# Performance work log

Hardware: AMD Instinct MI355X
Metric: run time of the kernel (lower is better)

## Reference

```python
import jax, jax.numpy as jnp
import numpy as np

DIM = 768
NUM_HEADS = 12
HEAD_DIM = DIM // NUM_HEADS
SCALE = HEAD_DIM ** -0.5
ELEV_SCALE = 1000.0


def setup_inputs() -> dict:
    key = jax.random.key(0)
    ks = jax.random.split(key, 6)
    B, N = 2, 2048
    x = jax.random.normal(ks[0], (B, N, DIM), dtype=jnp.float32)
    # elevation in meters, roughly 0..3000 m
    elevation_patches = jax.random.uniform(ks[1], (B, N), dtype=jnp.float32) * 3000.0
    # torch nn.Linear weights are [out, in]; y = x @ W.T + b
    w_qkv = jax.random.normal(ks[2], (3 * DIM, DIM), dtype=jnp.float32) * (DIM ** -0.5)
    w_proj = jax.random.normal(ks[3], (DIM, DIM), dtype=jnp.float32) * (DIM ** -0.5)
    b_proj = jax.random.normal(ks[4], (DIM,), dtype=jnp.float32) * 0.02
    alpha = jnp.ones((1,), dtype=jnp.float32)
    return {"x": x, "elevation_patches": elevation_patches,
            "w_qkv": w_qkv, "w_proj": w_proj, "b_proj": b_proj, "alpha": alpha}


def _elevation_bias(elev, alpha):
    # elev: [B, N] -> bias [B, N, N]; penalize uphill (elev_j > elev_i)
    diff = (elev[:, None, :] - elev[:, :, None]) / ELEV_SCALE  # [B, N, N]
    bias = -alpha[0] * jax.nn.relu(diff)
    return jnp.clip(bias, -10.0, 0.0)


def reference(x, elevation_patches, w_qkv, w_proj, b_proj, alpha):
    B, N, D = x.shape
    H, Hd = NUM_HEADS, HEAD_DIM
    qkv = x @ w_qkv.T                                   # [B, N, 3D]
    qkv = qkv.reshape(B, N, 3, H, Hd)
    q = jnp.transpose(qkv[:, :, 0], (0, 2, 1, 3))       # [B, H, N, Hd]
    k = jnp.transpose(qkv[:, :, 1], (0, 2, 1, 3))
    v = jnp.transpose(qkv[:, :, 2], (0, 2, 1, 3))
    scores = jnp.einsum('bhnd,bhmd->bhnm', q, k) * SCALE  # [B, H, N, N]
    bias = _elevation_bias(elevation_patches, alpha)       # [B, N, N]
    scores = scores + bias[:, None, :, :]
    attn = jax.nn.softmax(scores, axis=-1)
    out = jnp.einsum('bhnm,bhmd->bhnd', attn, v)           # [B, H, N, Hd]
    out = jnp.transpose(out, (0, 2, 1, 3)).reshape(B, N, D)
    return out @ w_proj.T + b_proj
```

## Files before the change

### kernel.cpp

```cpp
#include <hip/hip_runtime.h>


typedef __attribute__((ext_vector_type(8))) short bf16x8;
typedef __attribute__((ext_vector_type(4))) float f32x4;
typedef __attribute__((ext_vector_type(16))) float f32x16;

__device__ __forceinline__ unsigned short f2bf(float f) {
  unsigned int u = __builtin_bit_cast(unsigned int, f);
  u += 0x7fffu + ((u >> 16) & 1u);
  return (unsigned short)(u >> 16);
}

__device__ __forceinline__ unsigned cvtpk(float lo, float hi) {
  unsigned r;
  asm("v_cvt_pk_bf16_f32 %0, %1, %2" : "=v"(r) : "v"(lo), "v"(hi));
  return r;
}

__device__ __forceinline__ float exp2v(float x) {
  float r;
  asm("v_exp_f32 %0, %1" : "=v"(r) : "v"(x));
  return r;
}

__device__ __forceinline__ int sw8(int row) {
  return ((row ^ (row >> 3)) & 7) << 3;
}

__device__ __forceinline__ void gload16(const unsigned short* g, unsigned short* l) {
  __builtin_amdgcn_global_load_lds(
      (const __attribute__((address_space(1))) unsigned int*)g,
      (__attribute__((address_space(3))) unsigned int*)l, 16, 0, 0);
}

__global__ __launch_bounds__(256)
void cvt2_kernel(const float* __restrict__ a, unsigned short* __restrict__ ao, int na8,
                 const float* __restrict__ b, unsigned short* __restrict__ bo, int nb8) {
  int i = blockIdx.x * 256 + threadIdx.x;
  const float* src; unsigned short* dst;
  if (i < na8) { src = a; dst = ao; }
  else {
    i -= na8;
    if (i >= nb8) return;
    src = b; dst = bo;
  }
  const float4 f0 = ((const float4*)src)[i * 2];
  const float4 f1 = ((const float4*)src)[i * 2 + 1];
  uint4 v;
  v.x = cvtpk(f0.x, f0.y);
  v.y = cvtpk(f0.z, f0.w);
  v.z = cvtpk(f1.x, f1.y);
  v.w = cvtpk(f1.z, f1.w);
  ((uint4*)dst)[i] = v;
}

__global__ __launch_bounds__(256)
void gemm_a32_kernel(const float* __restrict__ Ap,
                     const unsigned short* __restrict__ Bp,
                     unsigned short* __restrict__ Cp, int M, int N, int K) {
  __shared__ __align__(16) unsigned short lds_a[2][128 * 32];
  __shared__ __align__(16) unsigned short lds_b[2][128 * 32];
  const int t = threadIdx.x;
  const int l = t & 63;
  const int w = t >> 6;
  const int wr = w >> 1, wc = w & 1;
  const int brow = blockIdx.x * 128;
  const int bcol = blockIdx.y * 128;
  const int l15 = l & 15, l4 = l >> 4;

  const int srow = t >> 2;
  const int scol = (t & 3) * 8;
  const float* ga = Ap + (size_t)(brow + srow) * K + scol;
  const unsigned short* gb = Bp + (size_t)(bcol + srow) * K + scol;

  f32x4 acc[4][4] = {};
  const int nk = K >> 5;

  float4 fa[4];
  {
    fa[0] = *(const float4*)ga;
    fa[1] = *(const float4*)(ga + 4);
    fa[2] = *(const float4*)(ga + (size_t)64 * K);
    fa[3] = *(const float4*)(ga + (size_t)64 * K + 4);
    unsigned short* lb = lds_b[0] + w * 512;
    gload16(gb, lb);
    gload16(gb + (size_t)64 * K, lb + 2048);
    uint4 u0, u1;
    u0.x = cvtpk(fa[0].x, fa[0].y); u0.y = cvtpk(fa[0].z, fa[0].w);
    u0.z = cvtpk(fa[1].x, fa[1].y); u0.w = cvtpk(fa[1].z, fa[1].w);
    u1.x = cvtpk(fa[2].x, fa[2].y); u1.y = cvtpk(fa[2].z, fa[2].w);
    u1.z = cvtpk(fa[3].x, fa[3].y); u1.w = cvtpk(fa[3].z, fa[3].w);
    *(uint4*)&lds_a[0][srow * 32 + scol] = u0;
    *(uint4*)&lds_a[0][(srow + 64) * 32 + scol] = u1;
  }
  __syncthreads();

  int buf = 0;
  for (int kt = 0; kt < nk; ++kt) {
    const bool more = kt + 1 < nk;
    if (more) {
      const size_t ko = (size_t)(kt + 1) * 32;
      fa[0] = *(const float4*)(ga + ko);
      fa[1] = *(const float4*)(ga + ko + 4);
      fa[2] = *(const float4*)(ga + ko + (size_t)64 * K);
      fa[3] = *(const float4*)(ga + ko + (size_t)64 * K + 4);
      unsigned short* lb = lds_b[buf ^ 1] + w * 512;
      gload16(gb + ko, lb);
      gload16(gb + ko + (size_t)64 * K, lb + 2048);
    }
    bf16x8 af[4], bfr[4];
#pragma unroll
    for (int i = 0; i < 4; ++i) {
      af[i]  = *(const bf16x8*)&lds_a[buf][(wr * 64 + i * 16 + l15) * 32 + l4 * 8];
      bfr[i] = *(const bf16x8*)&lds_b[buf][(wc * 64 + i * 16 + l15) * 32 + l4 * 8];
    }
#pragma unroll
    for (int i = 0; i < 4; ++i)
#pragma unroll
      for (int j = 0; j < 4; ++j)
        acc[i][j] = __builtin_amdgcn_mfma_f32_16x16x32_bf16(af[i], bfr[j], acc[i][j], 0, 0, 0);
    if (more) {
      uint4 u0, u1;
      u0.x = cvtpk(fa[0].x, fa[0].y); u0.y = cvtpk(fa[0].z, fa[0].w);
      u0.z = cvtpk(fa[1].x, fa[1].y); u0.w = cvtpk(fa[1].z, fa[1].w);
      u1.x = cvtpk(fa[2].x, fa[2].y); u1.y = cvtpk(fa[2].z, fa[2].w);
      u1.z = cvtpk(fa[3].x, fa[3].y); u1.w = cvtpk(fa[3].z, fa[3].w);
      *(uint4*)&lds_a[buf ^ 1][srow * 32 + scol] = u0;
      *(uint4*)&lds_a[buf ^ 1][(srow + 64) * 32 + scol] = u1;
    }
    __syncthreads();
    buf ^= 1;
  }

#pragma unroll
  for (int i = 0; i < 4; ++i)
#pragma unroll
    for (int j = 0; j < 4; ++j)
#pragma unroll
      for (int r = 0; r < 4; ++r) {
        const int row = brow + wr * 64 + i * 16 + l4 * 4 + r;
        const int col = bcol + wc * 64 + j * 16 + l15;
        Cp[(size_t)row * N + col] = f2bf(acc[i][j][r]);
      }
}

__global__ __launch_bounds__(256)
void gemm2_kernel(const unsigned short* __restrict__ Ap,
                  const unsigned short* __restrict__ Bp,
                  const float* __restrict__ bias, float* __restrict__ Cp,
                  int M, int N, int K) {
  __shared__ __align__(16) unsigned short lds_a[2][64 * 32];
  __shared__ __align__(16) unsigned short lds_b[2][128 * 32];
  const int t = threadIdx.x;
  const int l = t & 63;
  const int w = t >> 6;
  const int wr = w >> 1, wc = w & 1;
  const int brow = blockIdx.x * 64;
  const int bcol = blockIdx.y * 128;
  const int l15 = l & 15, l4 = l >> 4;

  const int srow = t >> 2;
  const int scol = (t & 3) * 8;
  const unsigned short* ga = Ap + (size_t)(brow + srow) * K + scol;
  const unsigned short* gb = Bp + (size_t)(bcol + srow) * K + scol;

  f32x4 acc[2][4] = {};
  const int nk = K >> 5;

  {
    gload16(ga, lds_a[0] + w * 512);
    unsigned short* lb = lds_b[0] + w * 512;
    gload16(gb, lb);
    gload16(gb + (size_t)64 * K, lb + 2048);
  }
  __syncthreads();

  int buf = 0;
  for (int kt = 0; kt < nk; ++kt) {
    if (kt + 1 < nk) {
      const size_t ko = (size_t)(kt + 1) * 32;
      gload16(ga + ko, lds_a[buf ^ 1] + w * 512);
      unsigned short* lb = lds_b[buf ^ 1] + w * 512;
      gload16(gb + ko, lb);
      gload16(gb + ko + (size_t)64 * K, lb + 2048);
    }
    bf16x8 af[2], bfr[4];
#pragma unroll
    for (int i = 0; i < 2; ++i)
      af[i] = *(const bf16x8*)&lds_a[buf][(wr * 32 + i * 16 + l15) * 32 + l4 * 8];
#pragma unroll
    for (int j = 0; j < 4; ++j)
      bfr[j] = *(const bf16x8*)&lds_b[buf][(wc * 64 + j * 16 + l15) * 32 + l4 * 8];
#pragma unroll
    for (int i = 0; i < 2; ++i)
#pragma unroll
      for (int j = 0; j < 4; ++j)
        acc[i][j] = __builtin_amdgcn_mfma_f32_16x16x32_bf16(af[i], bfr[j], acc[i][j], 0, 0, 0);
    __syncthreads();
    buf ^= 1;
  }

#pragma unroll
  for (int i = 0; i < 2; ++i)
#pragma unroll
    for (int j = 0; j < 4; ++j)
#pragma unroll
      for (int r = 0; r < 4; ++r) {
        const int row = brow + wr * 32 + i * 16 + l4 * 4 + r;
        const int col = bcol + wc * 64 + j * 16 + l15;
        Cp[(size_t)row * N + col] = acc[i][j][r] + bias[col];
      }
}

__global__ __launch_bounds__(512)
void attn_kernel(const unsigned short* __restrict__ qkv,
                 const float* __restrict__ elev,
                 const float* __restrict__ alpha_p,
                 unsigned short* __restrict__ aout) {
  __shared__ __align__(16) unsigned short lds_k[2][64 * 64];
  __shared__ __align__(16) unsigned short lds_vt[2][64 * 64];
  __shared__ __align__(16) float lds_ej[2][64];

  const int t = threadIdx.x;
  const int l = t & 63;
  const int w = t >> 6;
  const int l31 = l & 31;
  const int h = l >> 5;
  const int b = blockIdx.x / 12, hd = blockIdx.x % 12;
  const int q0 = blockIdx.y * 256 + w * 32;

  const float cE = fmaxf(alpha_p[0], 0.f) * (1.4426950408889634f * 1e-3f);
  const float c1 = 0.18033688011112042f;

  const size_t rs = 2304;
  const unsigned short* qbase = qkv + ((size_t)b * 2048) * rs + hd * 64;
  const unsigned short* kbase = qbase + 768;
  const unsigned short* vbase = qbase + 1536;

  bf16x8 qa[4];
  {
    const unsigned short* qp = qbase + (size_t)(q0 + l31) * rs + h * 8;
#pragma unroll
    for (int ks = 0; ks < 4; ++ks) qa[ks] = *(const bf16x8*)(qp + ks * 16);
  }
  const float eiv = elev[(size_t)b * 2048 + q0 + l31] * cE;

  uint4 onesu; onesu.x = onesu.y = onesu.z = onesu.w = 0x3F803F80u;
  const bf16x8 onesf = __builtin_bit_cast(bf16x8, onesu);

  f32x16 o[2] = {};
  f32x16 ps = {};

  const int sr = t >> 3;
  const int sc = (t & 7) * 8;

  uint4 rk, rv;
  float evn = 0.f;

  rk = *(const uint4*)(kbase + (size_t)sr * rs + sc);
  rv = *(const uint4*)(vbase + (size_t)sr * rs + sc);
  if (t < 64) evn = elev[(size_t)b * 2048 + t];
  *(uint4*)&lds_k[0][sr * 64 + (sc ^ sw8(sr))] = rk;
  {
    union { uint4 u; unsigned short s[8]; } vu; vu.u = rv;
#pragma unroll
    for (int j = 0; j < 8; ++j) {
      const int d = sc + j;
      lds_vt[0][d * 64 + (sr ^ sw8(d))] = vu.s[j];
    }
  }
  if (t < 64) lds_ej[0][t] = evn * cE;
  __syncthreads();

  for (int it = 0; it < 32; ++it) {
    const int cur = it & 1;
    const bool more = it < 31;
    if (more) {
      const int kv1 = (it + 1) * 64;
      rk = *(const uint4*)(kbase + (size_t)(kv1 + sr) * rs + sc);
      rv = *(const uint4*)(vbase + (size_t)(kv1 + sr) * rs + sc);
      if (t < 64) evn = elev[(size_t)b * 2048 + kv1 + t];
    }

    f32x16 st[2] = {};
    __builtin_amdgcn_s_setprio(1);
#pragma unroll
    for (int kst = 0; kst < 4; ++kst) {
      const int col = kst * 16 + h * 8;
#pragma unroll
      for (int mb = 0; mb < 2; ++mb) {
        const int row = mb * 32 + l31;
        bf16x8 kf = *(const bf16x8*)&lds_k[cur][row * 64 + (col ^ sw8(row))];
        st[mb] = __builtin_amdgcn_mfma_f32_32x32x16_bf16(kf, qa[kst], st[mb], 0, 0, 0);
      }
    }
    __builtin_amdgcn_s_setprio(0);

    bf16x8 pa[4];
#pragma unroll
    for (int mb = 0; mb < 2; ++mb) {
      float p16[16];
#pragma unroll
      for (int rr = 0; rr < 4; ++rr) {
        const float4 ejq = *(const float4*)&lds_ej[cur][mb * 32 + rr * 8 + h * 4];
#pragma unroll
        for (int jl = 0; jl < 4; ++jl) {
          const int r = rr * 4 + jl;
          const float bm = __builtin_amdgcn_fmed3f(ejq[jl] - eiv, 0.f, 14.4269504f);
          p16[r] = exp2v(__builtin_fmaf(st[mb][r], c1, -bm));
        }
      }
#pragma unroll
      for (int ks2 = 0; ks2 < 2; ++ks2) {
        unsigned u0 = cvtpk(p16[ks2 * 8 + 0], p16[ks2 * 8 + 1]);
        unsigned u1 = cvtpk(p16[ks2 * 8 + 2], p16[ks2 * 8 + 3]);
        unsigned v0 = cvtpk(p16[ks2 * 8 + 4], p16[ks2 * 8 + 5]);
        unsigned v1 = cvtpk(p16[ks2 * 8 + 6], p16[ks2 * 8 + 7]);
        asm volatile("v_permlane32_swap_b32 %0, %1" : "+v"(u0), "+v"(v0));
        asm volatile("v_permlane32_swap_b32 %0, %1" : "+v"(u1), "+v"(v1));
        uint4 fr; fr.x = u0; fr.y = u1; fr.z = v0; fr.w = v1;
        pa[mb * 2 + ks2] = __builtin_bit_cast(bf16x8, fr);
      }
    }

    __builtin_amdgcn_s_setprio(1);
#pragma unroll
    for (int ks = 0; ks < 4; ++ks) {
      const int col = ks * 16 + h * 8;
#pragma unroll
      for (int nb = 0; nb < 2; ++nb) {
        const int row = nb * 32 + l31;
        bf16x8 vf = *(const bf16x8*)&lds_vt[cur][row * 64 + (col ^ sw8(row))];
        o[nb] = __builtin_amdgcn_mfma_f32_32x32x16_bf16(pa[ks], vf, o[nb], 0, 0, 0);
      }
      ps = __builtin_amdgcn_mfma_f32_32x32x16_bf16(pa[ks], onesf, ps, 0, 0, 0);
    }
    __builtin_amdgcn_s_setprio(0);

    if (more) {
      const int nxt = cur ^ 1;
      *(uint4*)&lds_k[nxt][sr * 64 + (sc ^ sw8(sr))] = rk;
      union { uint4 u; unsigned short s[8]; } vu; vu.u = rv;
#pragma unroll
      for (int j = 0; j < 8; ++j) {
        const int d = sc + j;
        lds_vt[nxt][d * 64 + (sr ^ sw8(d))] = vu.s[j];
      }
      if (t < 64) lds_ej[nxt][t] = evn * cE;
    }
    __syncthreads();
  }

  float inv[16];
#pragma unroll
  for (int r = 0; r < 16; ++r) inv[r] = 1.0f / ps[r];
#pragma unroll
  for (int nb = 0; nb < 2; ++nb) {
    const int col = hd * 64 + nb * 32 + l31;
#pragma unroll
    for (int rr = 0; rr < 4; ++rr)
#pragma unroll
      for (int jl = 0; jl < 4; ++jl) {
        const int r = rr * 4 + jl;
        const int q = q0 + rr * 8 + h * 4 + jl;
        aout[((size_t)b * 2048 + q) * 768 + col] = f2bf(o[nb][r] * inv[r]);
      }
  }
}

extern "C" void kernel_launch(void* const* d_in, const int* in_sizes, int n_in,
                              void* d_out, int out_size, void* d_ws, size_t ws_size,
                              hipStream_t stream) {
  const float* x      = (const float*)d_in[0];
  const float* elev   = (const float*)d_in[1];
  const float* w_qkv  = (const float*)d_in[2];
  const float* w_proj = (const float*)d_in[3];
  const float* b_proj = (const float*)d_in[4];
  const float* alpha  = (const float*)d_in[5];
  float* out = (float*)d_out;

  unsigned short* qkvb   = (unsigned short*)d_ws;
  unsigned short* aob    = qkvb + (size_t)4096 * 2304;
  unsigned short* wqkvb  = aob + (size_t)4096 * 768;
  unsigned short* wprojb = wqkvb + (size_t)2304 * 768;

  cvt2_kernel<<<1152, 256, 0, stream>>>(w_qkv, wqkvb, 2304 * 768 / 8,
                                        w_proj, wprojb, 768 * 768 / 8);

  gemm_a32_kernel<<<dim3(32, 18), 256, 0, stream>>>(
      x, wqkvb, qkvb, 4096, 2304, 768);

  attn_kernel<<<dim3(24, 8), 512, 0, stream>>>(qkvb, elev, alpha, aob);

  gemm2_kernel<<<dim3(64, 6), 256, 0, stream>>>(
      aob, wprojb, b_proj, out, 4096, 768, 768);
}
```

Before: 100.5 us.

## Double attention KV tile to 128 rows and remap GEMM blocks per XCD

The attention kernel now stages 128 keys and values per iteration instead of 64. This halves the number of loop iterations and __syncthreads barriers, and gives the scheduler two independent score/softmax/PV chains per iteration to interleave. The GEMM kernel remaps block indices so that consecutive blocks on the same XCD share row tiles, aiming at better L2 reuse. The cost is doubled LDS use and higher register pressure from the extra score accumulators and prefetch registers, which may reduce occupancy.

Measured after the change: 102.6 us. 2.2% more time.

```diff
diff --git a/kernel.cpp b/kernel.cpp
--- a/kernel.cpp
+++ b/kernel.cpp
@@ -64,8 +64,11 @@
   const int l = t & 63;
   const int w = t >> 6;
   const int wr = w >> 1, wc = w & 1;
-  const int brow = blockIdx.x * 128;
-  const int bcol = blockIdx.y * 128;
+  const int bid = blockIdx.x + gridDim.x * blockIdx.y;
+  const int xcd = bid & 7;
+  const int idx = bid >> 3;
+  const int brow = (xcd * 4 + (idx & 3)) * 128;
+  const int bcol = (idx >> 2) * 128;
   const int l15 = l & 15, l4 = l >> 4;
 
   const int srow = t >> 2;
@@ -217,9 +220,9 @@
                  const float* __restrict__ elev,
                  const float* __restrict__ alpha_p,
                  unsigned short* __restrict__ aout) {
-  __shared__ __align__(16) unsigned short lds_k[2][64 * 64];
-  __shared__ __align__(16) unsigned short lds_vt[2][64 * 64];
-  __shared__ __align__(16) float lds_ej[2][64];
+  __shared__ __align__(16) unsigned short lds_k[2][128 * 64];
+  __shared__ __align__(16) unsigned short lds_vt[2][64 * 128];
+  __shared__ __align__(16) float lds_ej[2][128];
 
   const int t = threadIdx.x;
   const int l = t & 63;
@@ -254,35 +257,41 @@
   const int sr = t >> 3;
   const int sc = (t & 7) * 8;
 
-  uint4 rk, rv;
+  uint4 rk[2], rv[2];
   float evn = 0.f;
 
-  rk = *(const uint4*)(kbase + (size_t)sr * rs + sc);
-  rv = *(const uint4*)(vbase + (size_t)sr * rs + sc);
-  if (t < 64) evn = elev[(size_t)b * 2048 + t];
-  *(uint4*)&lds_k[0][sr * 64 + (sc ^ sw8(sr))] = rk;
-  {
-    union { uint4 u; unsigned short s[8]; } vu; vu.u = rv;
+  rk[0] = *(const uint4*)(kbase + (size_t)sr * rs + sc);
+  rk[1] = *(const uint4*)(kbase + (size_t)(sr + 64) * rs + sc);
+  rv[0] = *(const uint4*)(vbase + (size_t)sr * rs + sc);
+  rv[1] = *(const uint4*)(vbase + (size_t)(sr + 64) * rs + sc);
+  if (t < 128) evn = elev[(size_t)b * 2048 + t];
+#pragma unroll
+  for (int i = 0; i < 2; ++i) {
+    const int r = sr + i * 64;
+    *(uint4*)&lds_k[0][r * 64 + (sc ^ sw8(r))] = rk[i];
+    union { uint4 u; unsigned short s2[8]; } vu; vu.u = rv[i];
 #pragma unroll
     for (int j = 0; j < 8; ++j) {
       const int d = sc + j;
-      lds_vt[0][d * 64 + (sr ^ sw8(d))] = vu.s[j];
-    }
-  }
-  if (t < 64) lds_ej[0][t] = evn * cE;
+      lds_vt[0][d * 128 + (r ^ sw8(d))] = vu.s2[j];
+    }
+  }
+  if (t < 128) lds_ej[0][t] = evn * cE;
   __syncthreads();
 
-  for (int it = 0; it < 32; ++it) {
-    const int cur = it & 1;
-    const bool more = it < 31;
+  for (int s = 0; s < 16; ++s) {
+    const int cur = s & 1;
+    const bool more = s < 15;
     if (more) {
-      const int kv1 = (it + 1) * 64;
-      rk = *(const uint4*)(kbase + (size_t)(kv1 + sr) * rs + sc);
-      rv = *(const uint4*)(vbase + (size_t)(kv1 + sr) * rs + sc);
-      if (t < 64) evn = elev[(size_t)b * 2048 + kv1 + t];
-    }
-
-    f32x16 st[2] = {};
+      const int kvn = (s + 1) * 128;
+      rk[0] = *(const uint4*)(kbase + (size_t)(kvn + sr) * rs + sc);
+      rk[1] = *(const uint4*)(kbase + (size_t)(kvn + sr + 64) * rs + sc);
+      rv[0] = *(const uint4*)(vbase + (size_t)(kvn + sr) * rs + sc);
+      rv[1] = *(const uint4*)(vbase + (size_t)(kvn + sr + 64) * rs + sc);
+      if (t < 128) evn = elev[(size_t)b * 2048 + kvn + t];
+    }
+
+    f32x16 st0[2] = {}, st1[2] = {};
     __builtin_amdgcn_s_setprio(1);
 #pragma unroll
     for (int kst = 0; kst < 4; ++kst) {
@@ -291,12 +300,22 @@
       for (int mb = 0; mb < 2; ++mb) {
         const int row = mb * 32 + l31;
         bf16x8 kf = *(const bf16x8*)&lds_k[cur][row * 64 + (col ^ sw8(row))];
-        st[mb] = __builtin_amdgcn_mfma_f32_32x32x16_bf16(kf, qa[kst], st[mb], 0, 0, 0);
+        st0[mb] = __builtin_amdgcn_mfma_f32_32x32x16_bf16(kf, qa[kst], st0[mb], 0, 0, 0);
+      }
+    }
+#pragma unroll
+    for (int kst = 0; kst < 4; ++kst) {
+      const int col = kst * 16 + h * 8;
+#pragma unroll
+      for (int mb = 0; mb < 2; ++mb) {
+        const int row = 64 + mb * 32 + l31;
+        bf16x8 kf = *(const bf16x8*)&lds_k[cur][row * 64 + (col ^ sw8(row))];
+        st1[mb] = __builtin_amdgcn_mfma_f32_32x32x16_bf16(kf, qa[kst], st1[mb], 0, 0, 0);
       }
     }
     __builtin_amdgcn_s_setprio(0);
 
-    bf16x8 pa[4];
+    bf16x8 pa0[4], pa1[4];
 #pragma unroll
     for (int mb = 0; mb < 2; ++mb) {
       float p16[16];
@@ -307,7 +326,7 @@
         for (int jl = 0; jl < 4; ++jl) {
           const int r = rr * 4 + jl;
           const float bm = __builtin_amdgcn_fmed3f(ejq[jl] - eiv, 0.f, 14.4269504f);
-          p16[r] = exp2v(__builtin_fmaf(st[mb][r], c1, -bm));
+          p16[r] = exp2v(__builtin_fmaf(st0[mb][r], c1, -bm));
         }
       }
 #pragma unroll
@@ -319,34 +338,78 @@
         asm volatile("v_permlane32_swap_b32 %0, %1" : "+v"(u0), "+v"(v0));
         asm volatile("v_permlane32_swap_b32 %0, %1" : "+v"(u1), "+v"(v1));
         uint4 fr; fr.x = u0; fr.y = u1; fr.z = v0; fr.w = v1;
-        pa[mb * 2 + ks2] = __builtin_bit_cast(bf16x8, fr);
+        pa0[mb * 2 + ks2] = __builtin_bit_cast(bf16x8, fr);
       }
     }
 
     __builtin_amdgcn_s_setprio(1);
 #pragma unroll
     for (int ks = 0; ks < 4; ++ks) {
-      const int col = ks * 16 + h * 8;
+      const int colb = ks * 16 + h * 8;
 #pragma unroll
       for (int nb = 0; nb < 2; ++nb) {
         const int row = nb * 32 + l31;
-        bf16x8 vf = *(const bf16x8*)&lds_vt[cur][row * 64 + (col ^ sw8(row))];
-        o[nb] = __builtin_amdgcn_mfma_f32_32x32x16_bf16(pa[ks], vf, o[nb], 0, 0, 0);
-      }
-      ps = __builtin_amdgcn_mfma_f32_32x32x16_bf16(pa[ks], onesf, ps, 0, 0, 0);
+        bf16x8 vf = *(const bf16x8*)&lds_vt[cur][row * 128 + (colb ^ sw8(row))];
+        o[nb] = __builtin_amdgcn_mfma_f32_32x32x16_bf16(pa0[ks], vf, o[nb], 0, 0, 0);
+      }
+      ps = __builtin_amdgcn_mfma_f32_32x32x16_bf16(pa0[ks], onesf, ps, 0, 0, 0);
+    }
+    __builtin_amdgcn_s_setprio(0);
+
+#pragma unroll
+    for (int mb = 0; mb < 2; ++mb) {
+      float p16[16];
+#pragma unroll
+      for (int rr = 0; rr < 4; ++rr) {
+        const float4 ejq = *(const float4*)&lds_ej[cur][64 + mb * 32 + rr * 8 + h * 4];
+#pragma unroll
+        for (int jl = 0; jl < 4; ++jl) {
+          const int r = rr * 4 + jl;
+          const float bm = __builtin_amdgcn_fmed3f(ejq[jl] - eiv, 0.f, 14.4269504f);
+          p16[r] = exp2v(__builtin_fmaf(st1[mb][r], c1, -bm));
+        }
+      }
+#pragma unroll
+      for (int ks2 = 0; ks2 < 2; ++ks2) {
+        unsigned u0 = cvtpk(p16[ks2 * 8 + 0], p16[ks2 * 8 + 1]);
+        unsigned u1 = cvtpk(p16[ks2 * 8 + 2], p16[ks2 * 8 + 3]);
+        unsigned v0 = cvtpk(p16[ks2 * 8 + 4], p16[ks2 * 8 + 5]);
+        unsigned v1 = cvtpk(p16[ks2 * 8 + 6], p16[ks2 * 8 + 7]);
+        asm volatile("v_permlane32_swap_b32 %0, %1" : "+v"(u0), "+v"(v0));
+        asm volatile("v_permlane32_swap_b32 %0, %1" : "+v"(u1), "+v"(v1));
+        uint4 fr; fr.x = u0; fr.y = u1; fr.z = v0; fr.w = v1;
+        pa1[mb * 2 + ks2] = __builtin_bit_cast(bf16x8, fr);
+      }
+    }
+
+    __builtin_amdgcn_s_setprio(1);
+#pragma unroll
+    for (int ks = 0; ks < 4; ++ks) {
+      const int colb = 64 + ks * 16 + h * 8;
+#pragma unroll
+      for (int nb = 0; nb < 2; ++nb) {
+        const int row = nb * 32 + l31;
+        bf16x8 vf = *(const bf16x8*)&lds_vt[cur][row * 128 + (colb ^ sw8(row))];
+        o[nb] = __builtin_amdgcn_mfma_f32_32x32x16_bf16(pa1[ks], vf, o[nb], 0, 0, 0);
+      }
+      ps = __builtin_amdgcn_mfma_f32_32x32x16_bf16(pa1[ks], onesf, ps, 0, 0, 0);
     }
     __builtin_amdgcn_s_setprio(0);
 
     if (more) {
       const int nxt = cur ^ 1;
-      *(uint4*)&lds_k[nxt][sr * 64 + (sc ^ sw8(sr))] = rk;
-      union { uint4 u; unsigned short s[8]; } vu; vu.u = rv;
-#pragma unroll
-      for (int j = 0; j < 8; ++j) {
-        const int d = sc + j;
-        lds_vt[nxt][d * 64 + (sr ^ sw8(d))] = vu.s[j];
-      }
-      if (t < 64) lds_ej[nxt][t] = evn * cE;
+#pragma unroll
+      for (int i = 0; i < 2; ++i) {
+        const int r = sr + i * 64;
+        *(uint4*)&lds_k[nxt][r * 64 + (sc ^ sw8(r))] = rk[i];
+        union { uint4 u; unsigned short s2[8]; } vu; vu.u = rv[i];
+#pragma unroll
+        for (int j = 0; j < 8; ++j) {
+          const int d = sc + j;
+          lds_vt[nxt][d * 128 + (r ^ sw8(d))] = vu.s2[j];
+        }
+      }
+      if (t < 128) lds_ej[nxt][t] = evn * cE;
     }
     __syncthreads();
   }
```
